# Performance work log

Measured on AMD Instinct MI355X. Metric: run time of the kernel, lower is better.

Reference implementation:

```python
import jax, jax.numpy as jnp
import numpy as np

N = 100000   # nodes
E = 300000   # directed edges
NG = 4096    # graphs in batch
F_IN = 22
HID = 128


def setup_inputs() -> dict:
    key = jax.random.key(0)
    ks = jax.random.split(key, 32)
    s = 0.05
    inp = {
        "x": jax.random.normal(ks[0], (N, F_IN), jnp.float32),
        "edge_index": jax.random.randint(ks[1], (2, E), 0, N),
        "batch": jnp.sort(jax.random.randint(ks[2], (N,), 0, NG)),
        # GAT layer 1: 22 -> 4 heads x 32
        "W1": jax.random.normal(ks[3], (F_IN, HID), jnp.float32) * s,
        "as1": jax.random.normal(ks[4], (4, 32), jnp.float32) * s,
        "ad1": jax.random.normal(ks[5], (4, 32), jnp.float32) * s,
        "b1": jnp.zeros((HID,), jnp.float32),
        "g1": jnp.ones((HID,), jnp.float32),
        "be1": jnp.zeros((HID,), jnp.float32),
        # GAT layer 2: 128 -> 4 heads x 32
        "W2": jax.random.normal(ks[6], (HID, HID), jnp.float32) * s,
        "as2": jax.random.normal(ks[7], (4, 32), jnp.float32) * s,
        "ad2": jax.random.normal(ks[8], (4, 32), jnp.float32) * s,
        "b2": jnp.zeros((HID,), jnp.float32),
        "g2": jnp.ones((HID,), jnp.float32),
        "be2": jnp.zeros((HID,), jnp.float32),
        # GAT layer 3: 128 -> 1 head x 128
        "W3": jax.random.normal(ks[9], (HID, HID), jnp.float32) * s,
        "as3": jax.random.normal(ks[10], (1, HID), jnp.float32) * s,
        "ad3": jax.random.normal(ks[11], (1, HID), jnp.float32) * s,
        "b3": jnp.zeros((HID,), jnp.float32),
        "g3": jnp.ones((HID,), jnp.float32),
        "be3": jnp.zeros((HID,), jnp.float32),
        # MLP head
        "fw1": jax.random.normal(ks[12], (HID, 64), jnp.float32) * s,
        "fb1": jnp.zeros((64,), jnp.float32),
        "fw2": jax.random.normal(ks[13], (64, 1), jnp.float32) * s,
        "fb2": jnp.zeros((1,), jnp.float32),
    }
    return inp


def reference(x, edge_index, batch, W1, as1, ad1, b1, g1, be1,
              W2, as2, ad2, b2, g2, be2, W3, as3, ad3, b3, g3, be3,
              fw1, fb1, fw2, fb2):
    n = x.shape[0]
    sl = jnp.arange(n)
    src = jnp.concatenate([edge_index[0], sl])  # PyG GATConv adds self-loops
    dst = jnp.concatenate([edge_index[1], sl])

    def gat(h_in, W, a_s, a_d, b):
        H, C = a_s.shape
        h = (h_in @ W).reshape(n, H, C)                      # [N,H,C]
        al_s = jnp.einsum('nhc,hc->nh', h, a_s)              # per-node src score
        al_d = jnp.einsum('nhc,hc->nh', h, a_d)
        e = jax.nn.leaky_relu(al_s[src] + al_d[dst], 0.2)    # [Etot,H]
        emax = jax.ops.segment_max(e, dst, num_segments=n)
        ex = jnp.exp(e - emax[dst])
        den = jax.ops.segment_sum(ex, dst, num_segments=n)
        alpha = ex / (den[dst] + 1e-16)                       # segment softmax over in-edges
        msg = h[src] * alpha[:, :, None]                      # [Etot,H,C]
        out = jax.ops.segment_sum(msg, dst, num_segments=n)
        return out.reshape(n, H * C) + b

    def bn(h, g, be):
        m = h.mean(0)
        v = h.var(0)
        return (h - m) * jax.lax.rsqrt(v + 1e-5) * g + be

    h = jax.nn.relu(bn(gat(x, W1, as1, ad1, b1), g1, be1))
    h = jax.nn.relu(bn(gat(h, W2, as2, ad2, b2), g2, be2))
    h = jax.nn.relu(bn(gat(h, W3, as3, ad3, b3), g3, be3))

    # global mean pool over graphs
    s = jax.ops.segment_sum(h, batch, num_segments=NG)
    cnt = jax.ops.segment_sum(jnp.ones((n,), h.dtype), batch, num_segments=NG)
    pooled = s / jnp.maximum(cnt, 1.0)[:, None]

    z = jax.nn.relu(pooled @ fw1 + fb1)
    return z @ fw2 + fb2
```

## Files before the change

### kernel.cpp

```cpp
#include <hip/hip_runtime.h>

#define N_NODES 100000
#define N_EDGES 300000
#define N_ETOT  400000
#define NGRAPH  4096
#define HID     128
#define NBLK_SCAN 391
#define PNPB    32
#define STATS_BLOCKS 512
#define NSLICE  16

typedef __attribute__((ext_vector_type(8))) short short8;
typedef __attribute__((ext_vector_type(8))) ushort ushort8;
typedef __attribute__((ext_vector_type(4))) float f32x4;

__device__ __forceinline__ ushort f2bf(float f) {
    union { float f; unsigned u; } x; x.f = f;
    unsigned r = x.u + 0x7FFF + ((x.u >> 16) & 1);
    return (ushort)(r >> 16);
}

__device__ __forceinline__ float bf2f(ushort v) {
    union { unsigned u; float f; } t;
    t.u = ((unsigned)v) << 16;
    return t.f;
}

__device__ __forceinline__ float2 bf2f2(unsigned v) {
    union { unsigned u; float f; } lo, hi;
    lo.u = v << 16;
    hi.u = v & 0xFFFF0000u;
    return make_float2(lo.f, hi.f);
}

#define SETUP_W      36864
#define SETUP_SUMS   (SETUP_W + 3 * NSLICE * 256)
#define SETUP_CNTS   (SETUP_SUMS + N_NODES)
#define SETUP_TOT    (SETUP_CNTS + NGRAPH * HID + NGRAPH)
__global__ __launch_bounds__(256) void setup_kernel(
    const float* __restrict__ W1, const float* __restrict__ W2, const float* __restrict__ W3,
    ushort* __restrict__ Wt1, ushort* __restrict__ Wt2, ushort* __restrict__ Wt3,
    float* __restrict__ sums_base, int* __restrict__ counts,
    float* __restrict__ pooled)
{
    const int i = blockIdx.x * 256 + threadIdx.x;
    if (i < 16384) {
        int c = i >> 7, k = i & 127;
        Wt2[c * 128 + k] = f2bf(W2[k * 128 + c]);
    } else if (i < 32768) {
        int j = i - 16384; int c = j >> 7, k = j & 127;
        Wt3[c * 128 + k] = f2bf(W3[k * 128 + c]);
    } else if (i < SETUP_W) {
        int j = i - 32768; int c = j >> 5, k = j & 31;
        Wt1[c * 32 + k] = (k < 22) ? f2bf(W1[k * 128 + c]) : (ushort)0;
    } else if (i < SETUP_SUMS) {
        sums_base[i - SETUP_W] = 0.f;
    } else if (i < SETUP_CNTS) {
        counts[i - SETUP_SUMS] = 0;
    } else if (i < SETUP_TOT) {
        pooled[i - SETUP_CNTS] = 0.f;
    }
}

template<int K, bool PRE_BN, int HH, bool DX>
__global__ __launch_bounds__(256) void mfma_gemm_kernel(
    const ushort* __restrict__ Ab, const float* __restrict__ Af,
    const ushort* __restrict__ Wt,
    const float* __restrict__ sums, const float* __restrict__ g, const float* __restrict__ be,
    const float* __restrict__ avs, const float* __restrict__ avd,
    ushort* __restrict__ Cb, float* __restrict__ als, float* __restrict__ ald, int M)
{
    constexpr int SEGS = K / 8;
    constexpr int SSH  = (K == 128) ? 4 : 2;
    constexpr int SWM  = SEGS - 1;
    constexpr int NP   = SEGS / 2;
    constexpr int KT   = K / 32;

    __shared__ ushort Asm[128 * K];
    __shared__ ushort Bsm[128 * K];
    __shared__ float scsh[256];

    const int tid  = threadIdx.x;
    const int wave = tid >> 6;
    const int lane = tid & 63;
    const int ln   = lane & 15;
    const int quad = lane >> 4;
    const int wr0  = (wave >> 1) * 64;
    const int wc0  = (wave & 1) * 64;
    const int row0 = blockIdx.x * 128;

    short8 aR[NP], wR[NP];
    #pragma unroll
    for (int q = 0; q < NP; ++q) {
        const int chunk = tid + q * 256;
        const int r   = chunk >> SSH;
        const int seg = chunk & SWM;
        if constexpr (DX) {
            const int rr = min(row0 + r, N_NODES - 1);
            #pragma unroll
            for (int i = 0; i < 8; ++i) {
                const int c = seg * 8 + i;
                const float f = (c < 22) ? Af[(size_t)rr * 22 + c] : 0.f;
                aR[q][i] = (short)f2bf(f);
            }
        } else {
            aR[q] = *(const short8*)&Ab[(size_t)(row0 + r) * K + seg * 8];
        }
        wR[q] = *(const short8*)&Wt[(size_t)r * K + seg * 8];
    }
    if constexpr (PRE_BN) {
        if (tid < 128) {
            float s = 0.f, q2 = 0.f;
            for (int b = 0; b < NSLICE; ++b) {
                s  += sums[b * 256 + tid];
                q2 += sums[b * 256 + 128 + tid];
            }
            const float m  = s * (1.f / N_NODES);
            const float v  = q2 * (1.f / N_NODES) - m * m;
            const float sc = g[tid] * rsqrtf(v + 1e-5f);
            scsh[tid]       = sc;
            scsh[tid + 128] = be[tid] - m * sc;
        }
        __syncthreads();
        #pragma unroll
        for (int q = 0; q < NP; ++q) {
            const int seg = (tid + q * 256) & SWM;
            const int cc  = seg * 8;
            #pragma unroll
            for (int i = 0; i < 8; ++i) {
                float f = bf2f((ushort)aR[q][i]);
                f = fmaxf(f * scsh[cc + i] + scsh[128 + cc + i], 0.f);
                aR[q][i] = (short)f2bf(f);
            }
        }
    }
    #pragma unroll
    for (int q = 0; q < NP; ++q) {
        const int chunk = tid + q * 256;
        const int r   = chunk >> SSH;
        const int seg = chunk & SWM;
        const int sp  = seg ^ (r & SWM);
        *(short8*)&Asm[r * K + sp * 8] = aR[q];
        *(short8*)&Bsm[r * K + sp * 8] = wR[q];
    }
    __syncthreads();

    f32x4 acc[4][4] = {};
    #pragma unroll
    for (int kt = 0; kt < KT; ++kt) {
        short8 af[4], bf[4];
        #pragma unroll
        for (int i = 0; i < 4; ++i) {
            const int ra = wr0 + i * 16 + ln;
            const int ca = wc0 + i * 16 + ln;
            af[i] = *(const short8*)&Asm[ra * K + (((kt * 4 + quad) ^ (ra & SWM)) * 8)];
            bf[i] = *(const short8*)&Bsm[ca * K + (((kt * 4 + quad) ^ (ca & SWM)) * 8)];
        }
        #pragma unroll
        for (int tr = 0; tr < 4; ++tr)
            #pragma unroll
            for (int tc = 0; tc < 4; ++tc)
                acc[tr][tc] = __builtin_amdgcn_mfma_f32_16x16x32_bf16(
                    af[tr], bf[tc], acc[tr][tc], 0, 0, 0);
    }

    #pragma unroll
    for (int tr = 0; tr < 4; ++tr)
        #pragma unroll
        for (int rg = 0; rg < 4; ++rg) {
            const int gr = row0 + wr0 + tr * 16 + quad * 4 + rg;
            if (gr < M) {
                #pragma unroll
                for (int tc = 0; tc < 4; ++tc)
                    Cb[(size_t)gr * HID + wc0 + tc * 16 + ln] = f2bf(acc[tr][tc][rg]);
            }
        }

    __syncthreads();
    float* ps = (float*)Asm;
    float* pd = (float*)Bsm;
    #pragma unroll
    for (int tr = 0; tr < 4; ++tr)
      #pragma unroll
      for (int rg = 0; rg < 4; ++rg) {
        float sA = 0.f, sB = 0.f, dA = 0.f, dB = 0.f;
        #pragma unroll
        for (int tc = 0; tc < 4; ++tc) {
            const int col = wc0 + tc * 16 + ln;
            const float v = acc[tr][tc][rg];
            if (tc < 2) { sA += v * avs[col]; dA += v * avd[col]; }
            else        { sB += v * avs[col]; dB += v * avd[col]; }
        }
        #pragma unroll
        for (int m = 1; m < 16; m <<= 1) {
            sA += __shfl_xor(sA, m); sB += __shfl_xor(sB, m);
            dA += __shfl_xor(dA, m); dB += __shfl_xor(dB, m);
        }
        if (ln == 0) {
            const int rl = wr0 + tr * 16 + quad * 4 + rg;
            const int h0 = (wave & 1) * 2;
            ps[rl * 4 + h0] = sA; ps[rl * 4 + h0 + 1] = sB;
            pd[rl * 4 + h0] = dA; pd[rl * 4 + h0 + 1] = dB;
        }
      }
    __syncthreads();
    {
        const int r  = tid & 127;
        const int gr = row0 + r;
        if (gr < M) {
            if (tid < 128) {
                if (HH == 4) {
                    #pragma unroll
                    for (int h = 0; h < 4; ++h) als[gr * 4 + h] = ps[r * 4 + h];
                } else als[gr] = ps[r * 4] + ps[r * 4 + 1] + ps[r * 4 + 2] + ps[r * 4 + 3];
            } else {
                if (HH == 4) {
                    #pragma unroll
                    for (int h = 0; h < 4; ++h) ald[gr * 4 + h] = pd[r * 4 + h];
                } else ald[gr] = pd[r * 4] + pd[r * 4 + 1] + pd[r * 4 + 2] + pd[r * 4 + 3];
            }
        }
    }
}

__global__ void hist_kernel(const int* __restrict__ ei, int* __restrict__ counts) {
    int e = blockIdx.x * blockDim.x + threadIdx.x;
    if (e >= N_ETOT) return;
    int dst = (e < N_EDGES) ? ei[N_EDGES + e] : e - N_EDGES;
    atomicAdd(&counts[dst], 1);
}

__global__ __launch_bounds__(256) void scanA_kernel(
    const int* __restrict__ counts, int* __restrict__ rowptr, int* __restrict__ bsum)
{
    __shared__ int ls[256];
    const int t = threadIdx.x;
    const int i = blockIdx.x * 256 + t;
    const int v = (i < N_NODES) ? counts[i] : 0;
    ls[t] = v; __syncthreads();
    #pragma unroll
    for (int off = 1; off < 256; off <<= 1) {
        int add = (t >= off) ? ls[t - off] : 0;
        __syncthreads();
        ls[t] += add;
        __syncthreads();
    }
    if (i < N_NODES) rowptr[i] = ls[t] - v;
    if (t == 255) bsum[blockIdx.x] = ls[255];
}

__global__ __launch_bounds__(256) void scanC_kernel(
    int* __restrict__ rowptr, const int* __restrict__ bsum, int* __restrict__ cursor)
{
    __shared__ int red[256];
    const int t = threadIdx.x;
    int s = 0;
    for (int b = t; b < (int)blockIdx.x; b += 256) s += bsum[b];
    red[t] = s;
    __syncthreads();
    #pragma unroll
    for (int off = 128; off; off >>= 1) {
        if (t < off) red[t] += red[t + off];
        __syncthreads();
    }
    const int base = red[0];
    const int i = blockIdx.x * 256 + t;
    if (i < N_NODES) {
        const int v = rowptr[i] + base;
        rowptr[i] = v;
        cursor[i] = v;
    }
    if (i == 0) rowptr[N_NODES] = N_ETOT;
}

__global__ void scatter_kernel(const int* __restrict__ ei, int* __restrict__ cursor,
                               int* __restrict__ psrc)
{
    int e = blockIdx.x * blockDim.x + threadIdx.x;
    if (e >= N_ETOT) return;
    int src, dst;
    if (e < N_EDGES) { src = ei[e]; dst = ei[N_EDGES + e]; }
    else             { src = dst = e - N_EDGES; }
    int pos = atomicAdd(&cursor[dst], 1);
    psrc[pos] = src;
}

template<int HH>
__global__ __launch_bounds__(256) void agg_kernel(
    const ushort* __restrict__ H, const float* __restrict__ als,
    const float* __restrict__ ald, const int* __restrict__ rowptr,
    const int* __restrict__ psrc, ushort* __restrict__ Outb)
{
    const int tid   = threadIdx.x;
    const int w     = tid >> 6;
    const int lane  = tid & 63;
    const int grp   = lane >> 4;
    const int cl    = lane & 15;
    const int hd    = (HH == 4) ? (cl >> 2) : 0;
    const int nodeA = blockIdx.x * 8 + w * 2;
    const int nodeB = nodeA + 1;

    const int r0A = rowptr[nodeA];
    const int r1A = rowptr[nodeA + 1];
    const int r1B = rowptr[nodeB + 1];
    const float aldA = (HH == 4) ? ald[nodeA * 4 + hd] : ald[nodeA];
    const float aldB = (HH == 4) ? ald[nodeB * 4 + hd] : ald[nodeB];

    float denA = 0.f, denB = 0.f;
    float accA[8] = {}, accB[8] = {};
    int pA = r0A + grp;
    int pB = r1A + grp;
    while (pA < r1A || pB < r1B) {
        const bool aA = pA < r1A;
        const bool aB = pB < r1B;
        const int qA = aA ? pA : (r1A - 1);
        const int qB = aB ? pB : (r1B - 1);
        const int sA = psrc[qA];
        const int sB = psrc[qB];
        const float svA = (HH == 4) ? als[sA * 4 + hd] : als[sA];
        const float svB = (HH == 4) ? als[sB * 4 + hd] : als[sB];
        const uint4 hvA = *(const uint4*)&H[(size_t)sA * HID + cl * 8];
        const uint4 hvB = *(const uint4*)&H[(size_t)sB * HID + cl * 8];

        float vA = svA + aldA; vA = (vA > 0.f) ? vA : 0.2f * vA;
        float vB = svB + aldB; vB = (vB > 0.f) ? vB : 0.2f * vB;
        const float exA = aA ? __expf(vA) : 0.f;
        const float exB = aB ? __expf(vB) : 0.f;
        {
            const float2 h0 = bf2f2(hvA.x), h1 = bf2f2(hvA.y);
            const float2 h2 = bf2f2(hvA.z), h3 = bf2f2(hvA.w);
            accA[0] += exA * h0.x; accA[1] += exA * h0.y;
            accA[2] += exA * h1.x; accA[3] += exA * h1.y;
            accA[4] += exA * h2.x; accA[5] += exA * h2.y;
            accA[6] += exA * h3.x; accA[7] += exA * h3.y;
            denA += exA;
        }
        {
            const float2 h0 = bf2f2(hvB.x), h1 = bf2f2(hvB.y);
            const float2 h2 = bf2f2(hvB.z), h3 = bf2f2(hvB.w);
            accB[0] += exB * h0.x; accB[1] += exB * h0.y;
            accB[2] += exB * h1.x; accB[3] += exB * h1.y;
            accB[4] += exB * h2.x; accB[5] += exB * h2.y;
            accB[6] += exB * h3.x; accB[7] += exB * h3.y;
            denB += exB;
        }
        pA += 4; pB += 4;
    }
    #pragma unroll
    for (int m = 16; m < 64; m <<= 1) {
        denA += __shfl_xor(denA, m);
        denB += __shfl_xor(denB, m);
        #pragma unroll
        for (int i = 0; i < 8; ++i) {
            accA[i] += __shfl_xor(accA[i], m);
            accB[i] += __shfl_xor(accB[i], m);
        }
    }
    if (grp == 0) {
        const float inv = 1.f / (denA + 1e-16f);
        ushort8 o;
        #pragma unroll
        for (int i = 0; i < 8; ++i) o[i] = f2bf(accA[i] * inv);
        *(ushort8*)&Outb[(size_t)nodeA * HID + cl * 8] = o;
    } else if (grp == 1) {
        const float inv = 1.f / (denB + 1e-16f);
        ushort8 o;
        #pragma unroll
        for (int i = 0; i < 8; ++i) o[i] = f2bf(accB[i] * inv);
        *(ushort8*)&Outb[(size_t)nodeB * HID + cl * 8] = o;
    }
}

__global__ __launch_bounds__(256) void bn_stats_kernel(
    const ushort* __restrict__ X, float* __restrict__ sums_sl)
{
    __shared__ float ls[16][128], lq[16][128];
    const int tid = threadIdx.x;
    const int ro  = tid >> 4;
    const int ci  = tid & 15;
    const int c0  = ci * 8;
    const int rpb = (N_NODES + STATS_BLOCKS - 1) / STATS_BLOCKS;
    const int r0  = blockIdx.x * rpb;
    const int r1  = min(r0 + rpb, N_NODES);

    float s[8] = {}, q[8] = {};
    for (int r = r0 + ro; r < r1; r += 16) {
        const ushort8 v = *(const ushort8*)&X[(size_t)r * HID + c0];
        #pragma unroll
        for (int j = 0; j < 8; ++j) {
            const float f = bf2f(v[j]);
            s[j] += f; q[j] += f * f;
        }
    }
    #pragma unroll
    for (int j = 0; j < 8; ++j) { ls[ro][c0 + j] = s[j]; lq[ro][c0 + j] = q[j]; }
    __syncthreads();
    const int half = tid >> 7;
    const int c    = tid & 127;
    float acc = 0.f;
    if (half == 0) {
        #pragma unroll
        for (int k = 0; k < 16; ++k) acc += ls[k][c];
    } else {
        #pragma unroll
        for (int k = 0; k < 16; ++k) acc += lq[k][c];
    }
    atomicAdd(&sums_sl[(blockIdx.x & (NSLICE - 1)) * 256 + tid], acc);
}

__global__ __launch_bounds__(128) void bn_pool_kernel(
    const ushort* __restrict__ X,
    const float* __restrict__ sums, const float* __restrict__ g, const float* __restrict__ be,
    const int* __restrict__ batch, float* __restrict__ pooled, float* __restrict__ cnt)
{
    const int c = threadIdx.x;
    float s = 0.f, q2 = 0.f;
    for (int b = 0; b < NSLICE; ++b) {
        s  += sums[b * 256 + c];
        q2 += sums[b * 256 + 128 + c];
    }
    const float m  = s * (1.f / N_NODES);
    const float vv = q2 * (1.f / N_NODES) - m * m;
    const float sc = g[c] * rsqrtf(vv + 1e-5f);
    const float sh = be[c] - m * sc;

    const int n0 = blockIdx.x * PNPB;
    const int n1 = min(n0 + PNPB, N_NODES);
    int gcur = batch[n0];
    float acc = 0.f;
    int run = 0;
    for (int n = n0; n < n1; ++n) {
        const int gg = batch[n];
        if (gg != gcur) {
            atomicAdd(&pooled[(size_t)gcur * HID + c], acc);
            if (c == 0) atomicAdd(&cnt[gcur], (float)run);
            acc = 0.f; run = 0; gcur = gg;
        }
        const float v = bf2f(X[(size_t)n * HID + c]) * sc + sh;
        acc += fmaxf(v, 0.f);
        ++run;
    }
    atomicAdd(&pooled[(size_t)gcur * HID + c], acc);
    if (c == 0) atomicAdd(&cnt[gcur], (float)run);
}

__global__ __launch_bounds__(256) void mlp_kernel(
    const float* __restrict__ pooled, const float* __restrict__ cnt,
    const float* __restrict__ fw1, const float* __restrict__ fb1,
    const float* __restrict__ fw2, const float* __restrict__ fb2,
    float* __restrict__ out)
{
    __shared__ float w1[HID * 64];
    __shared__ float rows[4][HID];
    const int tid = threadIdx.x;
    for (int i = tid; i < HID * 64; i += 256) w1[i] = fw1[i];
    const int gl = tid >> 6;
    const int j  = tid & 63;
    const float b1 = fb1[j];
    const float w2 = fw2[j];
    __syncthreads();
    #pragma unroll
    for (int it = 0; it < 4; ++it) {
        const int g = blockIdx.x * 16 + it * 4 + gl;
        const float inv = 1.f / fmaxf(cnt[g], 1.f);
        rows[gl][j]      = pooled[(size_t)g * HID + j] * inv;
        rows[gl][j + 64] = pooled[(size_t)g * HID + 64 + j] * inv;
        __syncthreads();
        float z = b1;
        #pragma unroll 8
        for (int c2 = 0; c2 < HID; ++c2) z += rows[gl][c2] * w1[c2 * 64 + j];
        z = fmaxf(z, 0.f);
        float p = z * w2;
        #pragma unroll
        for (int off = 32; off; off >>= 1) p += __shfl_down(p, off);
        if (j == 0) out[g] = p + fb2[0];
        __syncthreads();
    }
}

extern "C" void kernel_launch(void* const* d_in, const int* in_sizes, int n_in,
                              void* d_out, int out_size, void* d_ws, size_t ws_size,
                              hipStream_t stream)
{
    const float* x     = (const float*)d_in[0];
    const int*   ei    = (const int*)d_in[1];
    const int*   batch = (const int*)d_in[2];
    const float* W1  = (const float*)d_in[3];
    const float* as1 = (const float*)d_in[4];
    const float* ad1 = (const float*)d_in[5];
    const float* g1  = (const float*)d_in[7];
    const float* be1 = (const float*)d_in[8];
    const float* W2  = (const float*)d_in[9];
    const float* as2 = (const float*)d_in[10];
    const float* ad2 = (const float*)d_in[11];
    const float* g2  = (const float*)d_in[13];
    const float* be2 = (const float*)d_in[14];
    const float* W3  = (const float*)d_in[15];
    const float* as3 = (const float*)d_in[16];
    const float* ad3 = (const float*)d_in[17];
    const float* g3  = (const float*)d_in[19];
    const float* be3 = (const float*)d_in[20];
    const float* fw1 = (const float*)d_in[21];
    const float* fb1 = (const float*)d_in[22];
    const float* fw2 = (const float*)d_in[23];
    const float* fb2 = (const float*)d_in[24];
    float* out = (float*)d_out;

    ushort* Hb  = (ushort*)d_ws;
    ushort* Bh  = Hb  + (size_t)N_NODES * HID;
    ushort* Wt1 = Bh  + (size_t)N_NODES * HID + 128 * 128;
    ushort* Wt2 = Wt1 + 128 * 32;
    ushort* Wt3 = Wt2 + 128 * 128;
    float* als    = (float*)(Wt3 + 128 * 128);
    float* ald    = als + (size_t)N_NODES * 4;
    float* sums1  = ald + (size_t)N_NODES * 4;
    float* sums2  = sums1 + NSLICE * 256;
    float* sums3  = sums2 + NSLICE * 256;
    float* pooled = sums3 + NSLICE * 256;
    float* cnt    = pooled + (size_t)NGRAPH * HID;
    int*   rowptr = (int*)(cnt + NGRAPH);
    int*   counts = rowptr + (N_NODES + 1);
    int*   cursor = counts + N_NODES;
    int*   bsum   = cursor + N_NODES;
    int*   psrc   = bsum + 512;

    auto cdiv = [](int a, int b) { return (a + b - 1) / b; };

    setup_kernel<<<cdiv(SETUP_TOT, 256), 256, 0, stream>>>(
        W1, W2, W3, Wt1, Wt2, Wt3, sums1, counts, pooled);

    hist_kernel<<<cdiv(N_ETOT, 256), 256, 0, stream>>>(ei, counts);
    scanA_kernel<<<NBLK_SCAN, 256, 0, stream>>>(counts, rowptr, bsum);
    scanC_kernel<<<NBLK_SCAN, 256, 0, stream>>>(rowptr, bsum, cursor);
    scatter_kernel<<<cdiv(N_ETOT, 256), 256, 0, stream>>>(ei, cursor, psrc);

    const int ggrid = cdiv(N_NODES, 128);
    const int agrid = N_NODES / 8;

    mfma_gemm_kernel<32, false, 4, true><<<ggrid, 256, 0, stream>>>(
        nullptr, x, Wt1, nullptr, nullptr, nullptr, as1, ad1, Hb, als, ald, N_NODES);
    agg_kernel<4><<<agrid, 256, 0, stream>>>(Hb, als, ald, rowptr, psrc, Bh);
    bn_stats_kernel<<<STATS_BLOCKS, 256, 0, stream>>>(Bh, sums1);

    mfma_gemm_kernel<128, true, 4, false><<<ggrid, 256, 0, stream>>>(
        Bh, nullptr, Wt2, sums1, g1, be1, as2, ad2, Hb, als, ald, N_NODES);
    agg_kernel<4><<<agrid, 256, 0, stream>>>(Hb, als, ald, rowptr, psrc, Bh);
    bn_stats_kernel<<<STATS_BLOCKS, 256, 0, stream>>>(Bh, sums2);

    mfma_gemm_kernel<128, true, 1, false><<<ggrid, 256, 0, stream>>>(
        Bh, nullptr, Wt3, sums2, g2, be2, as3, ad3, Hb, als, ald, N_NODES);
    agg_kernel<1><<<agrid, 256, 0, stream>>>(Hb, als, ald, rowptr, psrc, Bh);
    bn_stats_kernel<<<STATS_BLOCKS, 256, 0, stream>>>(Bh, sums3);

    bn_pool_kernel<<<cdiv(N_NODES, PNPB), 128, 0, stream>>>(
        Bh, sums3, g3, be3, batch, pooled, cnt);
    mlp_kernel<<<NGRAPH / 16, 256, 0, stream>>>(pooled, cnt, fw1, fb1, fw2, fb2, out);
}
```

Before: 338.0 us.

## Load A fragments directly into registers, one 16-row strip per wave

```diff
diff --git a/kernel.cpp b/kernel.cpp
--- a/kernel.cpp
+++ b/kernel.cpp
@@ -73,10 +73,9 @@
     constexpr int SEGS = K / 8;
     constexpr int SSH  = (K == 128) ? 4 : 2;
     constexpr int SWM  = SEGS - 1;
-    constexpr int NP   = SEGS / 2;
+    constexpr int NPB  = SEGS / 2;
     constexpr int KT   = K / 32;
 
-    __shared__ ushort Asm[128 * K];
     __shared__ ushort Bsm[128 * K];
     __shared__ float scsh[256];
 
@@ -85,28 +84,31 @@
     const int lane = tid & 63;
     const int ln   = lane & 15;
     const int quad = lane >> 4;
-    const int wr0  = (wave >> 1) * 64;
-    const int wc0  = (wave & 1) * 64;
-    const int row0 = blockIdx.x * 128;
-
-    short8 aR[NP], wR[NP];
-    #pragma unroll
-    for (int q = 0; q < NP; ++q) {
+    const int r0   = blockIdx.x * 64 + wave * 16;
+    const int ra   = r0 + ln;
+
+    short8 wR[NPB];
+    #pragma unroll
+    for (int q = 0; q < NPB; ++q) {
         const int chunk = tid + q * 256;
         const int r   = chunk >> SSH;
         const int seg = chunk & SWM;
+        wR[q] = *(const short8*)&Wt[(size_t)r * K + seg * 8];
+    }
+    short8 aF[KT];
+    #pragma unroll
+    for (int kt = 0; kt < KT; ++kt) {
         if constexpr (DX) {
-            const int rr = min(row0 + r, N_NODES - 1);
+            const int rr = min(ra, N_NODES - 1);
             #pragma unroll
             for (int i = 0; i < 8; ++i) {
-                const int c = seg * 8 + i;
+                const int c = kt * 32 + quad * 8 + i;
                 const float f = (c < 22) ? Af[(size_t)rr * 22 + c] : 0.f;
-                aR[q][i] = (short)f2bf(f);
+                aF[kt][i] = (short)f2bf(f);
             }
         } else {
-            aR[q] = *(const short8*)&Ab[(size_t)(row0 + r) * K + seg * 8];
-        }
-        wR[q] = *(const short8*)&Wt[(size_t)r * K + seg * 8];
+            aF[kt] = *(const short8*)&Ab[(size_t)ra * K + kt * 32 + quad * 8];
+        }
     }
     if constexpr (PRE_BN) {
         if (tid < 128) {
@@ -121,103 +123,88 @@
             scsh[tid]       = sc;
             scsh[tid + 128] = be[tid] - m * sc;
         }
-        __syncthreads();
-        #pragma unroll
-        for (int q = 0; q < NP; ++q) {
-            const int seg = (tid + q * 256) & SWM;
-            const int cc  = seg * 8;
-            #pragma unroll
-            for (int i = 0; i < 8; ++i) {
-                float f = bf2f((ushort)aR[q][i]);
-                f = fmaxf(f * scsh[cc + i] + scsh[128 + cc + i], 0.f);
-                aR[q][i] = (short)f2bf(f);
-            }
-        }
-    }
-    #pragma unroll
-    for (int q = 0; q < NP; ++q) {
+    }
+    #pragma unroll
+    for (int q = 0; q < NPB; ++q) {
         const int chunk = tid + q * 256;
         const int r   = chunk >> SSH;
         const int seg = chunk & SWM;
         const int sp  = seg ^ (r & SWM);
-        *(short8*)&Asm[r * K + sp * 8] = aR[q];
         *(short8*)&Bsm[r * K + sp * 8] = wR[q];
     }
     __syncthreads();
 
-    f32x4 acc[4][4] = {};
+    if constexpr (PRE_BN) {
+        #pragma unroll
+        for (int kt = 0; kt < KT; ++kt) {
+            const int c0 = kt * 32 + quad * 8;
+            #pragma unroll
+            for (int i = 0; i < 8; ++i) {
+                float f = bf2f((ushort)aF[kt][i]);
+                f = fmaxf(f * scsh[c0 + i] + scsh[128 + c0 + i], 0.f);
+                aF[kt][i] = (short)f2bf(f);
+            }
+        }
+    }
+
+    f32x4 acc[8] = {};
     #pragma unroll
     for (int kt = 0; kt < KT; ++kt) {
-        short8 af[4], bf[4];
-        #pragma unroll
-        for (int i = 0; i < 4; ++i) {
-            const int ra = wr0 + i * 16 + ln;
-            const int ca = wc0 + i * 16 + ln;
-            af[i] = *(const short8*)&Asm[ra * K + (((kt * 4 + quad) ^ (ra & SWM)) * 8)];
-            bf[i] = *(const short8*)&Bsm[ca * K + (((kt * 4 + quad) ^ (ca & SWM)) * 8)];
-        }
-        #pragma unroll
-        for (int tr = 0; tr < 4; ++tr)
+        #pragma unroll
+        for (int tc = 0; tc < 8; ++tc) {
+            const int ca = tc * 16 + ln;
+            const short8 b = *(const short8*)&Bsm[ca * K + (((kt * 4 + quad) ^ (ca & SWM)) * 8)];
+            acc[tc] = __builtin_amdgcn_mfma_f32_16x16x32_bf16(aF[kt], b, acc[tc], 0, 0, 0);
+        }
+    }
+
+    #pragma unroll
+    for (int rg = 0; rg < 4; ++rg) {
+        const int gr = r0 + quad * 4 + rg;
+        if (gr < M) {
             #pragma unroll
-            for (int tc = 0; tc < 4; ++tc)
-                acc[tr][tc] = __builtin_amdgcn_mfma_f32_16x16x32_bf16(
-                    af[tr], bf[tc], acc[tr][tc], 0, 0, 0);
-    }
-
-    #pragma unroll
-    for (int tr = 0; tr < 4; ++tr)
-        #pragma unroll
-        for (int rg = 0; rg < 4; ++rg) {
-            const int gr = row0 + wr0 + tr * 16 + quad * 4 + rg;
-            if (gr < M) {
+            for (int tc = 0; tc < 8; ++tc)
+                Cb[(size_t)gr * HID + tc * 16 + ln] = f2bf(acc[tc][rg]);
+        }
+    }
+
+    float avsr[8], avdr[8];
+    #pragma unroll
+    for (int tc = 0; tc < 8; ++tc) {
+        avsr[tc] = avs[tc * 16 + ln];
+        avdr[tc] = avd[tc * 16 + ln];
+    }
+    #pragma unroll
+    for (int rg = 0; rg < 4; ++rg) {
+        const int gr = r0 + quad * 4 + rg;
+        float s[4], d[4];
+        #pragma unroll
+        for (int h = 0; h < 4; ++h) {
+            float sv = 0.f, dv = 0.f;
+            sv += acc[2 * h][rg] * avsr[2 * h];
+            sv += acc[2 * h + 1][rg] * avsr[2 * h + 1];
+            dv += acc[2 * h][rg] * avdr[2 * h];
+            dv += acc[2 * h + 1][rg] * avdr[2 * h + 1];
+            s[h] = sv; d[h] = dv;
+        }
+        #pragma unroll
+        for (int m = 1; m < 16; m <<= 1) {
+            #pragma unroll
+            for (int h = 0; h < 4; ++h) {
+                s[h] += __shfl_xor(s[h], m);
+                d[h] += __shfl_xor(d[h], m);
+            }
+        }
+        if (ln == 0 && gr < M) {
+            if (HH == 4) {
                 #pragma unroll
-                for (int tc = 0; tc < 4; ++tc)
-                    Cb[(size_t)gr * HID + wc0 + tc * 16 + ln] = f2bf(acc[tr][tc][rg]);
-            }
-        }
-
-    __syncthreads();
-    float* ps = (float*)Asm;
-    float* pd = (float*)Bsm;
-    #pragma unroll
-    for (int tr = 0; tr < 4; ++tr)
-      #pragma unroll
-      for (int rg = 0; rg < 4; ++rg) {
-        float sA = 0.f, sB = 0.f, dA = 0.f, dB = 0.f;
-        #pragma unroll
-        for (int tc = 0; tc < 4; ++tc) {
-            const int col = wc0 + tc * 16 + ln;
-            const float v = acc[tr][tc][rg];
-            if (tc < 2) { sA += v * avs[col]; dA += v * avd[col]; }
-            else        { sB += v * avs[col]; dB += v * avd[col]; }
-        }
-        #pragma unroll
-        for (int m = 1; m < 16; m <<= 1) {
-            sA += __shfl_xor(sA, m); sB += __shfl_xor(sB, m);
-            dA += __shfl_xor(dA, m); dB += __shfl_xor(dB, m);
-        }
-        if (ln == 0) {
-            const int rl = wr0 + tr * 16 + quad * 4 + rg;
-            const int h0 = (wave & 1) * 2;
-            ps[rl * 4 + h0] = sA; ps[rl * 4 + h0 + 1] = sB;
-            pd[rl * 4 + h0] = dA; pd[rl * 4 + h0 + 1] = dB;
-        }
-      }
-    __syncthreads();
-    {
-        const int r  = tid & 127;
-        const int gr = row0 + r;
-        if (gr < M) {
-            if (tid < 128) {
-                if (HH == 4) {
-                    #pragma unroll
-                    for (int h = 0; h < 4; ++h) als[gr * 4 + h] = ps[r * 4 + h];
-                } else als[gr] = ps[r * 4] + ps[r * 4 + 1] + ps[r * 4 + 2] + ps[r * 4 + 3];
+                for (int h = 0; h < 4; ++h) {
+                    als[gr * 4 + h] = s[h];
+                    ald[gr * 4 + h] = d[h];
+                }
             } else {
-                if (HH == 4) {
-                    #pragma unroll
-                    for (int h = 0; h < 4; ++h) ald[gr * 4 + h] = pd[r * 4 + h];
-                } else ald[gr] = pd[r * 4] + pd[r * 4 + 1] + pd[r * 4 + 2] + pd[r * 4 + 3];
+                als[gr] = ((s[0] + s[1]) + s[2]) + s[3];
+                ald[gr] = ((d[0] + d[1]) + d[2]) + d[3];
             }
         }
     }
@@ -534,7 +521,7 @@
     scanC_kernel<<<NBLK_SCAN, 256, 0, stream>>>(rowptr, bsum, cursor);
     scatter_kernel<<<cdiv(N_ETOT, 256), 256, 0, stream>>>(ei, cursor, psrc);
 
-    const int ggrid = cdiv(N_NODES, 128);
+    const int ggrid = cdiv(N_NODES, 64);
     const int agrid = N_NODES / 8;
 
     mfma_gemm_kernel<32, false, 4, true><<<ggrid, 256, 0, stream>>>(
```

After: 322.0 us. 4.7% less time.
